# Kernel tuning notes

Measured on AMD Instinct MI355X. Metric: run time of the kernel, lower is better.

The kernel has to match this reference:

```python
import jax, jax.numpy as jnp
from jax import lax
import numpy as np

# Straight-through-estimator sign (standard BNN binarization):
# fwd: sign(x) with sign(0)=+1; bwd: pass gradient where |x|<=1 (hardtanh STE).
@jax.custom_vjp
def sign_ste(x):
    return jnp.where(x >= 0, 1.0, -1.0).astype(x.dtype)

def _sign_fwd(x):
    return sign_ste(x), x

def _sign_bwd(x, g):
    return (g * (jnp.abs(x) <= 1.0).astype(g.dtype),)

sign_ste.defvjp(_sign_fwd, _sign_bwd)

EPS = 1e-5  # BatchNorm eps (torch default)

def bn4(x, g, b):  # BatchNorm2d, training-mode batch stats, x: [N,C,H,W]
    m = x.mean((0, 2, 3), keepdims=True)
    v = x.var((0, 2, 3), keepdims=True)
    return g[None, :, None, None] * (x - m) * lax.rsqrt(v + EPS) + b[None, :, None, None]

def bn1(x, g, b):  # BatchNorm1d, x: [N,C]
    m = x.mean(0, keepdims=True)
    v = x.var(0, keepdims=True)
    return g * (x - m) * lax.rsqrt(v + EPS) + b

def bconv(x, W, b, first):
    # BinarizedConv2d: binarize weights always; binarize input except first layer.
    xb = x if first else sign_ste(x)
    y = lax.conv_general_dilated(xb, sign_ste(W), (1, 1), [(1, 1), (1, 1)],
                                 dimension_numbers=('NCHW', 'OIHW', 'NCHW'))
    return y + b[None, :, None, None]

def maxpool2(x):
    return lax.reduce_window(x, -jnp.inf, lax.max, (1, 1, 2, 2), (1, 1, 2, 2), 'VALID')

def ht(x):  # Hardtanh
    return jnp.clip(x, -1.0, 1.0)

CONV_CH = [(3, 64), (64, 128), (128, 256), (256, 256), (256, 512), (512, 512), (512, 512), (512, 512)]
LIN_CH = [(512, 512), (512, 512), (512, 10)]
POOL_AFTER = (0, 1, 3, 5, 7)  # conv indices followed by MaxPool2d

def setup_inputs():
    key = jax.random.key(0)
    ks = iter(jax.random.split(key, 64))
    d = {"x": jax.random.normal(next(ks), (256, 3, 32, 32), jnp.float32)}
    for i, (ci, co) in enumerate(CONV_CH):
        d[f"cw{i}"] = jax.random.normal(next(ks), (co, ci, 3, 3), jnp.float32) * 0.1
        d[f"cb{i}"] = jnp.zeros((co,), jnp.float32)
        d[f"cg{i}"] = jnp.ones((co,), jnp.float32)
        d[f"ct{i}"] = jnp.zeros((co,), jnp.float32)
    for i, (ci, co) in enumerate(LIN_CH):
        d[f"lw{i}"] = jax.random.normal(next(ks), (co, ci), jnp.float32) * 0.1
        d[f"lb{i}"] = jnp.zeros((co,), jnp.float32)
        d[f"lg{i}"] = jnp.ones((co,), jnp.float32)
        d[f"lt{i}"] = jnp.zeros((co,), jnp.float32)
    return d

def _forward(x, cw, cb, cg, ct, lw, lb, lg, lt):
    h = x
    for i in range(8):
        h = bconv(h, cw[i], cb[i], i == 0)
        if i in POOL_AFTER:
            h = maxpool2(h)
        h = ht(bn4(h, cg[i], ct[i]))
    h = h.reshape(h.shape[0], -1)  # [N, 512] after 5 pools on 32x32
    for i in range(3):
        h = sign_ste(h) @ sign_ste(lw[i]).T + lb[i]  # BinarizedLinear
        h = bn1(h, lg[i], lt[i])
        if i < 2:
            h = ht(h)  # Dropout is identity in eval mode
    return jax.nn.log_softmax(h, axis=-1)

def reference(x,
              cw0, cb0, cg0, ct0, cw1, cb1, cg1, ct1, cw2, cb2, cg2, ct2,
              cw3, cb3, cg3, ct3, cw4, cb4, cg4, ct4, cw5, cb5, cg5, ct5,
              cw6, cb6, cg6, ct6, cw7, cb7, cg7, ct7,
              lw0, lb0, lg0, lt0, lw1, lb1, lg1, lt1, lw2, lb2, lg2, lt2):
    cw = [cw0, cw1, cw2, cw3, cw4, cw5, cw6, cw7]
    cb = [cb0, cb1, cb2, cb3, cb4, cb5, cb6, cb7]
    cg = [cg0, cg1, cg2, cg3, cg4, cg5, cg6, cg7]
    ct = [ct0, ct1, ct2, ct3, ct4, ct5, ct6, ct7]
    lw = [lw0, lw1, lw2]
    lb = [lb0, lb1, lb2]
    lg = [lg0, lg1, lg2]
    lt = [lt0, lt1, lt2]
    return _forward(x, cw, cb, cg, ct, lw, lb, lg, lt)
```

## Files before the change

### kernel.cpp

```cpp
#include <hip/hip_runtime.h>
#include <hip/hip_bf16.h>

typedef unsigned long long u64;

#define EPSV 1e-5

__device__ __forceinline__ int imax(int a, int b) { return a > b ? a : b; }
__device__ __forceinline__ int iclamp(int v, int lo, int hi) { return v < lo ? lo : (v > hi ? hi : v); }

struct PrepArgs {
    const float* src[10];
    u64* dst[10];
    int CW[10];
    int Co[10];
    int taps[10];
    int rowbase[11];
    u64* accs;
    int naccs;
};

__global__ __launch_bounds__(256) void prep_kernel(PrepArgs a) {
    __shared__ float buf[4608];
    const int blk = blockIdx.x;
    int z = blk * 19 + threadIdx.x;
    if (threadIdx.x < 19 && z < a.naccs) a.accs[z] = 0ULL;

    int l = 0;
    while (l < 9 && blk >= a.rowbase[l + 1]) ++l;
    const int row = blk - a.rowbase[l];
    const int CW = a.CW[l];
    const int taps = a.taps[l];
// ... 86 lines not shown
        double t1 = 0.0, t2 = 0.0;
#pragma unroll
        for (int r = 0; r < 4; ++r) { t1 += sh1[r][threadIdx.x]; t2 += sh2[r][threadIdx.x]; }
        double* sh = dacc + (size_t)(blockIdx.x & 7) * 1024;
        atomicAdd(&sh[2 * threadIdx.x], t1);
        atomicAdd(&sh[2 * threadIdx.x + 1], t2);
    }
}

__global__ __launch_bounds__(256) void bnpack_i(const short* __restrict__ in,
                                                const u64* __restrict__ iacc,
                                                const float* __restrict__ g,
                                                const float* __restrict__ b,
                                                u64* __restrict__ act, int Co, int wshift,
                                                int count) {
    __shared__ int2 sthr[520];
    for (int i = threadIdx.x; i < Co; i += 256) {
        long long S1 = 0, S2 = 0;
#pragma unroll
        for (int s = 0; s < 8; ++s) {
            S1 += (long long)iacc[s * 1024 + 2 * i];
            S2 += (long long)iacc[s * 1024 + 2 * i + 1];
        }
        double m = (double)S1 / count;
        double var = (double)S2 / count - m * m;
        double sc = (double)g[i] / sqrt(var + EPSV);
        int2 r;
        if (sc == 0.0) r = make_int2(b[i] >= 0.f ? (int)0x80000000 : 0x7fffffff, 0);
        else {
            double t = m - (double)b[i] / sc;
            if (t > 1.0e9) t = 1.0e9;
            if (t < -1.0e9) t = -1.0e9;
            r = (sc > 0.0) ? make_int2((int)ceil(t), 0) : make_int2((int)floor(t), 1);
        }
        sthr[(i >> 6) * 65 + (i & 63)] = r;
    }
    __syncthreads();
    int tid = blockIdx.x * 256 + threadIdx.x;
    int part = tid & 3;
    int word = tid >> 2;
    int w = word & ((1 << wshift) - 1);
    int pix = word >> wshift;
    const int4* r4 = (const int4*)(in + (size_t)pix * Co + (w << 6) + part * 16);
    u64 bits = 0;
#pragma unroll
    for (int q = 0; q < 2; ++q) {
        int4 v = r4[q];
        int words4[4] = {v.x, v.y, v.z, v.w};
#pragma unroll
        for (int u = 0; u < 4; ++u) {
#pragma unroll
            for (int h = 0; h < 2; ++h) {
                int c = part * 16 + q * 8 + u * 2 + h;
                int val = (int)(short)((h == 0) ? (words4[u] & 0xffff) : ((unsigned)words4[u] >> 16));
                int2 t = sthr[w * 65 + c];
                bool bit = t.y ? (val <= t.x) : (val >= t.x);
                bits |= (u64)bit << c;
            }
        }
    }
    bits |= __shfl_xor(bits, 1);
    bits |= __shfl_xor(bits, 2);
    if (part == 0) act[word] = bits;
}

template <int CW, int HIN, bool POOL, int WC, bool INTERIOR>
__device__ __forceinline__ void row_accum(const u64* __restrict__ inb,
                                          const u64* __restrict__ wpkT, int Co, int co,
                                          const int* yoff, const bool* ry, int* cnt) {
    constexpr int HP = POOL ? HIN / 2 : HIN;
    constexpr int WS = POOL ? 4 : 3;
    constexpr int NA = POOL ? 4 : 1;
#pragma unroll 1
    for (int w0 = 0; w0 < CW; w0 += WC) {
        u64 wg[9 * WC];
#pragma unroll
        for (int k = 0; k < 9; ++k)
#pragma unroll
            for (int w = 0; w < WC; ++w)
                wg[k * WC + w] = wpkT[(size_t)(k * CW + w0 + w) * Co + co];
        u64 cur[WS][WS][WC];
#pragma unroll
        for (int d = 0; d < WS; ++d) {
            int cc = d - 1;
            int ccc = cc < 0 ? 0 : cc;
#pragma unroll
            for (int r = 0; r < WS; ++r) {
                const u64* p = inb + yoff[r] + ccc * CW + w0;
                if (WC == 1) {
                    cur[r][d][0] = p[0];
                } else {
                    ulonglong2 v = *(const ulonglong2*)p;
                    cur[r][d][0] = v.x;
                    cur[r][d][1] = v.y;
                }
            }
        }
#pragma unroll
        for (int xp = 0; xp < HP; ++xp) {
            if constexpr (POOL) {
#pragma unroll
                for (int py = 0; py < 2; ++py)
#pragma unroll
                    for (int qx = 0; qx < 2; ++qx)
#pragma unroll
                        for (int ky = 0; ky < 3; ++ky)
#pragma unroll
                            for (int kx = 0; kx < 3; ++kx) {
                                int d = qx + kx;
                                int cc = 2 * xp + d - 1;
                                if (cc >= 0 && cc < HIN) {
#pragma unroll
                                    for (int w = 0; w < WC; ++w) {
                                        int pc = (int)__popcll(cur[py + ky][d][w] ^
                                                               wg[(ky * 3 + kx) * WC + w]);
                                        if constexpr (INTERIOR)
                                            cnt[xp * NA + py * 2 + qx] += pc;
                                        else
                                            cnt[xp * NA + py * 2 + qx] += ry[py + ky] ? pc : 0;
                                    }
                                }
                            }
            } else {
#pragma unroll
                for (int ky = 0; ky < 3; ++ky)
#pragma unroll
                    for (int kx = 0; kx < 3; ++kx) {
                        int cc = xp + kx - 1;
                        if (cc >= 0 && cc < HIN) {
#pragma unroll
                            for (int w = 0; w < WC; ++w) {
                                int pc = (int)__popcll(cur[ky][kx][w] ^
                                                       wg[(ky * 3 + kx) * WC + w]);
                                if constexpr (INTERIOR)
                                    cnt[xp] += pc;
                                else
                                    cnt[xp] += ry[ky] ? pc : 0;
                            }
                        }
                    }
            }
            if (xp < HP - 1) {
                if constexpr (POOL) {
#pragma unroll
                    for (int r = 0; r < WS; ++r)
#pragma unroll
                        for (int w = 0; w < WC; ++w) {
                            cur[r][0][w] = cur[r][2][w];
                            cur[r][1][w] = cur[r][3][w];
                        }
#pragma unroll
                    for (int dd = 2; dd < 4; ++dd) {
                        int cc = 2 * (xp + 1) + dd - 1;
                        int ccc = cc >= HIN ? HIN - 1 : cc;
#pragma unroll
                        for (int r = 0; r < WS; ++r) {
                            const u64* p = inb + yoff[r] + ccc * CW + w0;
                            if (WC == 1) {
                                cur[r][dd][0] = p[0];
                            } else {
                                ulonglong2 v = *(const ulonglong2*)p;
                                cur[r][dd][0] = v.x;
                                cur[r][dd][1] = v.y;
                            }
                        }
                    }
                } else {
#pragma unroll
                    for (int r = 0; r < WS; ++r)
#pragma unroll
                        for (int w = 0; w < WC; ++w) {
                            cur[r][0][w] = cur[r][1][w];
                            cur[r][1][w] = cur[r][2][w];
                        }
                    int cc = xp + 2;
                    int ccc = cc >= HIN ? HIN - 1 : cc;
#pragma unroll
                    for (int r = 0; r < WS; ++r) {
                        const u64* p = inb + yoff[r] + ccc * CW + w0;
                        if (WC == 1) {
                            cur[r][2][0] = p[0];
                        } else {
                            ulonglong2 v = *(const ulonglong2*)p;
                            cur[r][2][0] = v.x;
                            cur[r][2][1] = v.y;
                        }
                    }
                }
            }
        }
    }
}

template <int CW, int HIN, bool POOL, int WC, bool FIRST>
__global__ __launch_bounds__(256) void bconv_row_f(const void* __restrict__ inprev,
                                                   const void* __restrict__ pstats,
                                                   const float* __restrict__ pg,
                                                   const float* __restrict__ pb, int pcount,
                                                   const u64* __restrict__ wpkT,
                                                   short* __restrict__ out,
                                                   u64* __restrict__ iacc, int Co) {
    constexpr int HP = POOL ? HIN / 2 : HIN;
    constexpr int WS = POOL ? 4 : 3;
    constexpr int NA = POOL ? 4 : 1;
    constexpr int ROWS = POOL ? 10 : 6;
    constexpr int Ci = CW * 64;
    __shared__ __align__(16) u64 sU[ROWS * HIN * CW];
    __shared__ int2 sthr[CW * 65];
    __shared__ float2 sthf[64];

    if constexpr (FIRST) {
        if (threadIdx.x < 64) {
            const double* dacc = (const double*)pstats;
            int i = threadIdx.x;
// ... 3 lines not shown
                S1 += dacc[s * 1024 + 2 * i];
                S2 += dacc[s * 1024 + 2 * i + 1];
            }
            double m = S1 / pcount;
            double var = S2 / pcount - m * m;
            double sc = (double)pg[i] / sqrt(var + EPSV);
            float2 r;
            if (sc == 0.0) r = make_float2(pb[i] >= 0.f ? -3.0e38f : 3.0e38f, 1.f);
            else {
                double t = m - (double)pb[i] / sc;
                r = make_float2((float)t, sc > 0.0 ? 1.f : -1.f);
            }
            sthf[i] = r;
        }
    } else {
        const u64* pacc = (const u64*)pstats;
        for (int i = threadIdx.x; i < Ci; i += 256) {
            long long S1 = 0, S2 = 0;
#pragma unroll
            for (int s = 0; s < 8; ++s) {
                S1 += (long long)pacc[s * 1024 + 2 * i];
                S2 += (long long)pacc[s * 1024 + 2 * i + 1];
            }
            double m = (double)S1 / pcount;
            double var = (double)S2 / pcount - m * m;
            double sc = (double)pg[i] / sqrt(var + EPSV);
            int2 r;
            if (sc == 0.0) r = make_int2(pb[i] >= 0.f ? (int)0x80000000 : 0x7fffffff, 0);
            else {
                double t = m - (double)pb[i] / sc;
                if (t > 1.0e9) t = 1.0e9;
                if (t < -1.0e9) t = -1.0e9;
                r = (sc > 0.0) ? make_int2((int)ceil(t), 0) : make_int2((int)floor(t), 1);
            }
            sthr[(i >> 6) * 65 + (i & 63)] = r;
        }
    }
    __syncthreads();

    const int bi = blockIdx.x;
    constexpr int BPN = HP / 4;
    const int n = bi / BPN;
    const int yp0 = (bi % BPN) * 4;
    const int ylo = imax(0, (POOL ? 2 * yp0 : yp0) - 1);
    const int yhiU = POOL ? (2 * yp0 + 8) : (yp0 + 4);
    const int yhi = yhiU > HIN - 1 ? HIN - 1 : yhiU;
    const int nrows = yhi - ylo + 1;
    const int nw = nrows * HIN * CW;

    if constexpr (FIRST) {
        const float* src = (const float*)inprev;
        for (int t = threadIdx.x; t < nw; t += 256) {
            int x = t % HIN;
            int yr = t / HIN;
            int y = ylo + yr;
            const float4* p = (const float4*)(src + (size_t)((n * 16 + y) * 16 + x) * 64);
            u64 bits = 0;
#pragma unroll
// ... 111 lines not shown
}

template <int CW, int HIN, bool POOL>
__global__ __launch_bounds__(256) void bconv_tiny_f(const short* __restrict__ inprev,
                                                    const u64* __restrict__ pacc,
                                                    const float* __restrict__ pg,
                                                    const float* __restrict__ pb, int pcount,
                                                    const u64* __restrict__ wpkT,
                                                    short* __restrict__ out,
                                                    u64* __restrict__ iacc, int Co) {
    constexpr int NPX = HIN * HIN;
    constexpr int HP = POOL ? HIN / 2 : HIN;
    constexpr int Ci = CW * 64;
    __shared__ int2 sthr[CW * 65];
    __shared__ u64 sU[4][NPX * CW];

    for (int i = threadIdx.x; i < Ci; i += 256) {
        long long S1 = 0, S2 = 0;
#pragma unroll
        for (int s = 0; s < 8; ++s) {
            S1 += (long long)pacc[s * 1024 + 2 * i];
            S2 += (long long)pacc[s * 1024 + 2 * i + 1];
        }
        double m = (double)S1 / pcount;
        double var = (double)S2 / pcount - m * m;
        double sc = (double)pg[i] / sqrt(var + EPSV);
        int2 r;
        if (sc == 0.0) r = make_int2(pb[i] >= 0.f ? (int)0x80000000 : 0x7fffffff, 0);
        else {
            double t = m - (double)pb[i] / sc;
            if (t > 1.0e9) t = 1.0e9;
            if (t < -1.0e9) t = -1.0e9;
            r = (sc > 0.0) ? make_int2((int)ceil(t), 0) : make_int2((int)floor(t), 1);
        }
        sthr[(i >> 6) * 65 + (i & 63)] = r;
    }
    __syncthreads();

    const int nbase = blockIdx.x * 4;
    for (int t = threadIdx.x; t < 4 * NPX * CW; t += 256) {
        int img = t / (NPX * CW);
        int rem = t % (NPX * CW);
        int w = rem % CW;
        int i = rem / CW;
        const int4* p = (const int4*)(inprev + (size_t)((nbase + img) * NPX + i) * Ci + w * 64);
        u64 bits = 0;
#pragma unroll
        for (int q = 0; q < 8; ++q) {
            int4 v = p[q];
            int wd[4] = {v.x, v.y, v.z, v.w};
#pragma unroll
            for (int u = 0; u < 4; ++u) {
#pragma unroll
                for (int h = 0; h < 2; ++h) {
                    int j = q * 8 + u * 2 + h;
                    int val = (int)(short)((h == 0) ? (wd[u] & 0xffff) : ((unsigned)wd[u] >> 16));
                    int2 th = sthr[w * 65 + j];
                    bool bit = th.y ? (val <= th.x) : (val >= th.x);
// ... 153 lines not shown
    __syncthreads();
    float z[10];
#pragma unroll
    for (int o = 0; o < 10; ++o) {
        double S1 = w1[0][o] + w1[1][o] + w1[2][o] + w1[3][o];
        double S2 = w2[0][o] + w2[1][o] + w2[2][o] + w2[3][o];
        double m = S1 / 256.0;
        double var = S2 / 256.0 - m * m;
        float sm = (float)m;
        float siv = (float)(1.0 / sqrt(var + EPSV));
        z[o] = g[o] * (v[o] - sm) * siv + bta[o];
    }
    float mx = z[0];
#pragma unroll
    for (int o = 1; o < 10; ++o) mx = fmaxf(mx, z[o]);
    float se = 0.f;
#pragma unroll
    for (int o = 0; o < 10; ++o) se += expf(z[o] - mx);
    float ls = logf(se);
#pragma unroll
    for (int o = 0; o < 10; ++o) out[n * 10 + o] = z[o] - mx - ls;
}

extern "C" void kernel_launch(void* const* d_in, const int* in_sizes, int n_in, void* d_out,
                              int out_size, void* d_ws, size_t ws_size, hipStream_t stream) {
    (void)in_sizes; (void)n_in; (void)out_size; (void)ws_size;
    const float* x = (const float*)d_in[0];
    const float *cw[8], *cb[8], *cg[8], *ct[8];
    for (int i = 0; i < 8; ++i) {
        cw[i] = (const float*)d_in[1 + 4 * i];
        cb[i] = (const float*)d_in[2 + 4 * i];
        cg[i] = (const float*)d_in[3 + 4 * i];
        ct[i] = (const float*)d_in[4 + 4 * i];
    }
    const float *lw[3], *lb[3], *lg[3], *lt[3];
    for (int i = 0; i < 3; ++i) {
        lw[i] = (const float*)d_in[33 + 4 * i];
        lb[i] = (const float*)d_in[34 + 4 * i];
        lg[i] = (const float*)d_in[35 + 4 * i];
        lt[i] = (const float*)d_in[36 + 4 * i];
    }

    static const int CIs[8] = {3, 64, 128, 256, 256, 512, 512, 512};
    static const int COs[8] = {64, 128, 256, 256, 512, 512, 512, 512};

    char* ws = (char*)d_ws;
    size_t off = 0;
    auto alloc = [&](size_t bytes) -> void* {
        void* p = ws + off;
        off += (bytes + 255) & ~(size_t)255;
        return p;
    };

    u64* accs = (u64*)alloc((size_t)8 * 8 * 1024 * 8);
    u64* fcs0 = (u64*)alloc(2048 * 8);
    u64* fcs1 = (u64*)alloc(2048 * 8);
    double* dacc0 = (double*)accs;
    auto iacc = [&](int layer) { return accs + (size_t)layer * 8192; };

    u64* wpkT[8] = {};
    for (int i = 1; i < 8; ++i) wpkT[i] = (u64*)alloc((size_t)COs[i] * 9 * (CIs[i] / 64) * 8);
    u64* wpl[3];
    int LO[3] = {512, 512, 10};
    for (int i = 0; i < 3; ++i) wpl[i] = (u64*)alloc((size_t)LO[i] * 8 * 8);
    u64* act7 = (u64*)alloc((size_t)256 * 8 * 8);
    float* out0 = (float*)alloc((size_t)65536 * 64 * 4);
    short* i16A = (short*)alloc((size_t)16384 * 256 * 2);
    short* i16B = (short*)alloc((size_t)16384 * 256 * 2);

    PrepArgs pa;
    int rb = 0;
    for (int i = 1; i < 8; ++i) {
        int e = i - 1;
        pa.src[e] = cw[i];
        pa.dst[e] = wpkT[i];
        pa.CW[e] = CIs[i] / 64;
        pa.Co[e] = COs[i];
        pa.taps[e] = 9;
        pa.rowbase[e] = rb;
        rb += COs[i];
    }
    for (int i = 0; i < 3; ++i) {
        int e = 7 + i;
        pa.src[e] = lw[i];
        pa.dst[e] = wpl[i];
        pa.CW[e] = 8;
        pa.Co[e] = LO[i];
        pa.taps[e] = 1;
        pa.rowbase[e] = rb;
        rb += LO[i];
    }
    pa.rowbase[10] = rb;
    pa.accs = accs;
    pa.naccs = 8 * 8 * 1024 + 2048 + 2048;
    prep_kernel<<<rb, 256, 0, stream>>>(pa);

    conv0_lane<<<2048, 256, 0, stream>>>(x, cw[0], out0, dacc0);

    bconv_row_f<1, 16, true, 1, true><<<dim3(512, 2), 256, 0, stream>>>(
        out0, dacc0, cg[0], ct[0], 65536, wpkT[1], i16A, iacc(1), 128);

    bconv_row_f<2, 8, false, 2, false><<<dim3(512, 4), 256, 0, stream>>>(
        i16A, iacc(1), cg[1], ct[1], 16384, wpkT[2], i16B, iacc(2), 256);

    bconv_row_f<4, 8, true, 2, false><<<dim3(256, 4), 256, 0, stream>>>(
        i16B, iacc(2), cg[2], ct[2], 16384, wpkT[3], i16A, iacc(3), 256);

    bconv_row_f<4, 4, false, 2, false><<<dim3(256, 8), 256, 0, stream>>>(
        i16A, iacc(3), cg[3], ct[3], 4096, wpkT[4], i16B, iacc(4), 512);

    bconv_tiny_f<8, 4, true><<<dim3(64, 8), 256, 0, stream>>>(
        i16B, iacc(4), cg[4], ct[4], 4096, wpkT[5], i16A, iacc(5), 512);

    bconv_tiny_f<8, 2, false><<<dim3(64, 8), 256, 0, stream>>>(
        i16A, iacc(5), cg[5], ct[5], 1024, wpkT[6], i16B, iacc(6), 512);

    bconv_tiny_f<8, 2, true><<<dim3(64, 8), 256, 0, stream>>>(
        i16B, iacc(6), cg[6], ct[6], 1024, wpkT[7], i16A, iacc(7), 512);

    bnpack_i<<<32, 256, 0, stream>>>(i16A, iacc(7), cg[7], ct[7], act7, 512, 3, 256);

    lin_kernel<<<512, 256, 0, stream>>>(act7, wpl[0], lb[0], lg[0], lt[0], fcs0);
    lin_kernel<<<512, 256, 0, stream>>>(fcs0, wpl[1], lb[1], lg[1], lt[1], fcs1);
    lin2_lsm<<<1, 256, 0, stream>>>(fcs1, wpl[2], lb[2], lg[2], lt[2], (float*)d_out);
}
```

Measured before the change: 405.9 us.

## Fuse all layer kernels into one cooperative persistent mega-kernel with grid syncs

Replaces the chain of about a dozen kernel launches (weight prep, conv layers, bn-pack, linear layers, log-softmax) with a single cooperative kernel. It loops persistent blocks over virtual tiles and uses grid-wide syncs between stages, keeping the old launch sequence as a fallback. The goal is to remove per-launch overhead and the idle tails between stages. In exchange, the grid is capped at 512 blocks sized by occupancy, which can leave big layers under-parallelized, and grid sync has its own cost. The 128-bit vector loads in row_accum are also replaced with two scalar loads.

```diff
diff --git a/kernel.cpp b/kernel.cpp
--- a/kernel.cpp
+++ b/kernel.cpp
@@ -1,5 +1,7 @@
 #include <hip/hip_runtime.h>
-#include <hip/hip_bf16.h>
+#include <hip/hip_cooperative_groups.h>
+
+namespace cg = cooperative_groups;
 
 typedef unsigned long long u64;
 
@@ -7,6 +9,147 @@
 
 __device__ __forceinline__ int imax(int a, int b) { return a > b ? a : b; }
 __device__ __forceinline__ int iclamp(int v, int lo, int hi) { return v < lo ? lo : (v > hi ? hi : v); }
+
+__device__ __forceinline__ int2 thr_int(long long S1, long long S2, float gv, float bv, int count) {
+    double m = (double)S1 / count;
+    double var = (double)S2 / count - m * m;
+    double sc = (double)gv / sqrt(var + EPSV);
+    int2 r;
+    if (sc == 0.0) r = make_int2(bv >= 0.f ? (int)0x80000000 : 0x7fffffff, 0);
+    else {
+        double t = m - (double)bv / sc;
+        if (t > 1.0e9) t = 1.0e9;
+        if (t < -1.0e9) t = -1.0e9;
+        r = (sc > 0.0) ? make_int2((int)ceil(t), 0) : make_int2((int)floor(t), 1);
+    }
+    return r;
+}
+
+template <int CW, int HIN, bool POOL, int WC, bool INTERIOR>
+__device__ __forceinline__ void row_accum(const u64* __restrict__ inb,
+                                          const u64* __restrict__ wpkT, int Co, int co,
+                                          const int* yoff, const bool* ry, int* cnt) {
+    constexpr int HP = POOL ? HIN / 2 : HIN;
+    constexpr int WS = POOL ? 4 : 3;
+    constexpr int NA = POOL ? 4 : 1;
+#pragma unroll 1
+    for (int w0 = 0; w0 < CW; w0 += WC) {
+        u64 wg[9 * WC];
+#pragma unroll
+        for (int k = 0; k < 9; ++k)
+#pragma unroll
+            for (int w = 0; w < WC; ++w)
+                wg[k * WC + w] = wpkT[(size_t)(k * CW + w0 + w) * Co + co];
+        u64 cur[WS][WS][WC];
+#pragma unroll
+        for (int d = 0; d < WS; ++d) {
+            int cc = d - 1;
+            int ccc = cc < 0 ? 0 : cc;
+#pragma unroll
+            for (int r = 0; r < WS; ++r) {
+                const u64* p = inb + yoff[r] + ccc * CW + w0;
+                if (WC == 1) {
+                    cur[r][d][0] = p[0];
+                } else {
+                    cur[r][d][0] = p[0];
+                    cur[r][d][1] = p[1];
+                }
+            }
+        }
+#pragma unroll
+        for (int xp = 0; xp < HP; ++xp) {
+            if constexpr (POOL) {
+#pragma unroll
+                for (int py = 0; py < 2; ++py)
+#pragma unroll
+                    for (int qx = 0; qx < 2; ++qx)
+#pragma unroll
+                        for (int ky = 0; ky < 3; ++ky)
+#pragma unroll
+                            for (int kx = 0; kx < 3; ++kx) {
+                                int d = qx + kx;
+                                int cc = 2 * xp + d - 1;
+                                if (cc >= 0 && cc < HIN) {
+#pragma unroll
+                                    for (int w = 0; w < WC; ++w) {
+                                        int pc = (int)__popcll(cur[py + ky][d][w] ^
+                                                               wg[(ky * 3 + kx) * WC + w]);
+                                        if constexpr (INTERIOR)
+                                            cnt[xp * NA + py * 2 + qx] += pc;
+                                        else
+                                            cnt[xp * NA + py * 2 + qx] += ry[py + ky] ? pc : 0;
+                                    }
+                                }
+                            }
+            } else {
+#pragma unroll
+                for (int ky = 0; ky < 3; ++ky)
+#pragma unroll
+                    for (int kx = 0; kx < 3; ++kx) {
+                        int cc = xp + kx - 1;
+                        if (cc >= 0 && cc < HIN) {
+#pragma unroll
+                            for (int w = 0; w < WC; ++w) {
+                                int pc = (int)__popcll(cur[ky][kx][w] ^
+                                                       wg[(ky * 3 + kx) * WC + w]);
+                                if constexpr (INTERIOR)
+                                    cnt[xp] += pc;
+                                else
+                                    cnt[xp] += ry[ky] ? pc : 0;
+                            }
+                        }
+                    }
+            }
+            if (xp < HP - 1) {
+                if constexpr (POOL) {
+#pragma unroll
+                    for (int r = 0; r < WS; ++r)
+#pragma unroll
+                        for (int w = 0; w < WC; ++w) {
+                            cur[r][0][w] = cur[r][2][w];
+                            cur[r][1][w] = cur[r][3][w];
+                        }
+#pragma unroll
+                    for (int dd = 2; dd < 4; ++dd) {
+                        int cc = 2 * (xp + 1) + dd - 1;
+                        int ccc = cc >= HIN ? HIN - 1 : cc;
+#pragma unroll
+                        for (int r = 0; r < WS; ++r) {
+                            const u64* p = inb + yoff[r] + ccc * CW + w0;
+                            if (WC == 1) {
+                                cur[r][dd][0] = p[0];
+                            } else {
+                                cur[r][dd][0] = p[0];
+                                cur[r][dd][1] = p[1];
+                            }
+                        }
+                    }
+                } else {
+#pragma unroll
+                    for (int r = 0; r < WS; ++r)
+#pragma unroll
+                        for (int w = 0; w < WC; ++w) {
+                            cur[r][0][w] = cur[r][1][w];
+                            cur[r][1][w] = cur[r][2][w];
+                        }
+                    int cc = xp + 2;
+                    int ccc = cc >= HIN ? HIN - 1 : cc;
+#pragma unroll
+                    for (int r = 0; r < WS; ++r) {
+                        const u64* p = inb + yoff[r] + ccc * CW + w0;
+                        if (WC == 1) {
+                            cur[r][2][0] = p[0];
+                        } else {
+                            cur[r][2][0] = p[0];
+                            cur[r][2][1] = p[1];
+                        }
+                    }
+                }
+            }
+        }
+    }
+}
+
 
 struct PrepArgs {
     const float* src[10];
@@ -139,18 +282,7 @@
             S1 += (long long)iacc[s * 1024 + 2 * i];
             S2 += (long long)iacc[s * 1024 + 2 * i + 1];
         }
-        double m = (double)S1 / count;
-        double var = (double)S2 / count - m * m;
-        double sc = (double)g[i] / sqrt(var + EPSV);
-        int2 r;
-        if (sc == 0.0) r = make_int2(b[i] >= 0.f ? (int)0x80000000 : 0x7fffffff, 0);
-        else {
-            double t = m - (double)b[i] / sc;
-            if (t > 1.0e9) t = 1.0e9;
-            if (t < -1.0e9) t = -1.0e9;
-            r = (sc > 0.0) ? make_int2((int)ceil(t), 0) : make_int2((int)floor(t), 1);
-        }
-        sthr[(i >> 6) * 65 + (i & 63)] = r;
+        sthr[(i >> 6) * 65 + (i & 63)] = thr_int(S1, S2, g[i], b[i], count);
     }
     __syncthreads();
     int tid = blockIdx.x * 256 + threadIdx.x;
@@ -179,134 +311,6 @@
     bits |= __shfl_xor(bits, 1);
     bits |= __shfl_xor(bits, 2);
     if (part == 0) act[word] = bits;
-}
-
-template <int CW, int HIN, bool POOL, int WC, bool INTERIOR>
-__device__ __forceinline__ void row_accum(const u64* __restrict__ inb,
-                                          const u64* __restrict__ wpkT, int Co, int co,
-                                          const int* yoff, const bool* ry, int* cnt) {
-    constexpr int HP = POOL ? HIN / 2 : HIN;
-    constexpr int WS = POOL ? 4 : 3;
-    constexpr int NA = POOL ? 4 : 1;
-#pragma unroll 1
-    for (int w0 = 0; w0 < CW; w0 += WC) {
-        u64 wg[9 * WC];
-#pragma unroll
-        for (int k = 0; k < 9; ++k)
-#pragma unroll
-            for (int w = 0; w < WC; ++w)
-                wg[k * WC + w] = wpkT[(size_t)(k * CW + w0 + w) * Co + co];
-        u64 cur[WS][WS][WC];
-#pragma unroll
-        for (int d = 0; d < WS; ++d) {
-            int cc = d - 1;
-            int ccc = cc < 0 ? 0 : cc;
-#pragma unroll
-            for (int r = 0; r < WS; ++r) {
-                const u64* p = inb + yoff[r] + ccc * CW + w0;
-                if (WC == 1) {
-                    cur[r][d][0] = p[0];
-                } else {
-                    ulonglong2 v = *(const ulonglong2*)p;
-                    cur[r][d][0] = v.x;
-                    cur[r][d][1] = v.y;
-                }
-            }
-        }
-#pragma unroll
-        for (int xp = 0; xp < HP; ++xp) {
-            if constexpr (POOL) {
-#pragma unroll
-                for (int py = 0; py < 2; ++py)
-#pragma unroll
-                    for (int qx = 0; qx < 2; ++qx)
-#pragma unroll
-                        for (int ky = 0; ky < 3; ++ky)
-#pragma unroll
-                            for (int kx = 0; kx < 3; ++kx) {
-                                int d = qx + kx;
-                                int cc = 2 * xp + d - 1;
-                                if (cc >= 0 && cc < HIN) {
-#pragma unroll
-                                    for (int w = 0; w < WC; ++w) {
-                                        int pc = (int)__popcll(cur[py + ky][d][w] ^
-                                                               wg[(ky * 3 + kx) * WC + w]);
-                                        if constexpr (INTERIOR)
-                                            cnt[xp * NA + py * 2 + qx] += pc;
-                                        else
-                                            cnt[xp * NA + py * 2 + qx] += ry[py + ky] ? pc : 0;
-                                    }
-                                }
-                            }
-            } else {
-#pragma unroll
-                for (int ky = 0; ky < 3; ++ky)
-#pragma unroll
-                    for (int kx = 0; kx < 3; ++kx) {
-                        int cc = xp + kx - 1;
-                        if (cc >= 0 && cc < HIN) {
-#pragma unroll
-                            for (int w = 0; w < WC; ++w) {
-                                int pc = (int)__popcll(cur[ky][kx][w] ^
-                                                       wg[(ky * 3 + kx) * WC + w]);
-                                if constexpr (INTERIOR)
-                                    cnt[xp] += pc;
-                                else
-                                    cnt[xp] += ry[ky] ? pc : 0;
-                            }
-                        }
-                    }
-            }
-            if (xp < HP - 1) {
-                if constexpr (POOL) {
-#pragma unroll
-                    for (int r = 0; r < WS; ++r)
-#pragma unroll
-                        for (int w = 0; w < WC; ++w) {
-                            cur[r][0][w] = cur[r][2][w];
-                            cur[r][1][w] = cur[r][3][w];
-                        }
-#pragma unroll
-                    for (int dd = 2; dd < 4; ++dd) {
-                        int cc = 2 * (xp + 1) + dd - 1;
-                        int ccc = cc >= HIN ? HIN - 1 : cc;
-#pragma unroll
-                        for (int r = 0; r < WS; ++r) {
-                            const u64* p = inb + yoff[r] + ccc * CW + w0;
-                            if (WC == 1) {
-                                cur[r][dd][0] = p[0];
-                            } else {
-                                ulonglong2 v = *(const ulonglong2*)p;
-                                cur[r][dd][0] = v.x;
-                                cur[r][dd][1] = v.y;
-                            }
-                        }
-                    }
-                } else {
-#pragma unroll
-                    for (int r = 0; r < WS; ++r)
-#pragma unroll
-                        for (int w = 0; w < WC; ++w) {
-                            cur[r][0][w] = cur[r][1][w];
-                            cur[r][1][w] = cur[r][2][w];
-                        }
-                    int cc = xp + 2;
-                    int ccc = cc >= HIN ? HIN - 1 : cc;
-#pragma unroll
-                    for (int r = 0; r < WS; ++r) {
-                        const u64* p = inb + yoff[r] + ccc * CW + w0;
-                        if (WC == 1) {
-                            cur[r][2][0] = p[0];
-                        } else {
-                            ulonglong2 v = *(const ulonglong2*)p;
-                            cur[r][2][0] = v.x;
-                            cur[r][2][1] = v.y;
-                        }
-                    }
-                }
-            }
-        }
-    }
 }
 
 template <int CW, int HIN, bool POOL, int WC, bool FIRST>
@@ -356,18 +360,7 @@
                 S1 += (long long)pacc[s * 1024 + 2 * i];
                 S2 += (long long)pacc[s * 1024 + 2 * i + 1];
             }
-            double m = (double)S1 / pcount;
-            double var = (double)S2 / pcount - m * m;
-            double sc = (double)pg[i] / sqrt(var + EPSV);
-            int2 r;
-            if (sc == 0.0) r = make_int2(pb[i] >= 0.f ? (int)0x80000000 : 0x7fffffff, 0);
-            else {
-                double t = m - (double)pb[i] / sc;
-                if (t > 1.0e9) t = 1.0e9;
-                if (t < -1.0e9) t = -1.0e9;
-                r = (sc > 0.0) ? make_int2((int)ceil(t), 0) : make_int2((int)floor(t), 1);
-            }
-            sthr[(i >> 6) * 65 + (i & 63)] = r;
+            sthr[(i >> 6) * 65 + (i & 63)] = thr_int(S1, S2, pg[i], pb[i], pcount);
         }
     }
     __syncthreads();
@@ -525,18 +518,7 @@
             S1 += (long long)pacc[s * 1024 + 2 * i];
             S2 += (long long)pacc[s * 1024 + 2 * i + 1];
         }
-        double m = (double)S1 / pcount;
-        double var = (double)S2 / pcount - m * m;
-        double sc = (double)pg[i] / sqrt(var + EPSV);
-        int2 r;
-        if (sc == 0.0) r = make_int2(pb[i] >= 0.f ? (int)0x80000000 : 0x7fffffff, 0);
-        else {
-            double t = m - (double)pb[i] / sc;
-            if (t > 1.0e9) t = 1.0e9;
-            if (t < -1.0e9) t = -1.0e9;
-            r = (sc > 0.0) ? make_int2((int)ceil(t), 0) : make_int2((int)floor(t), 1);
-        }
-        sthr[(i >> 6) * 65 + (i & 63)] = r;
+        sthr[(i >> 6) * 65 + (i & 63)] = thr_int(S1, S2, pg[i], pb[i], pcount);
     }
     __syncthreads();
 
@@ -736,14 +718,636 @@
     for (int o = 0; o < 10; ++o) out[n * 10 + o] = z[o] - mx - ls;
 }
 
+
+struct MegaArgs {
+    const float* psrc[10];
+    u64* pdst[10];
+    int pCW[10];
+    int pCo[10];
+    int ptaps[10];
+    int prow[11];
+    u64* accs;
+    int naccs;
+    const float* x;
+    const float* cw0;
+    float* out0;
+    const float* cg[8];
+    const float* ct[8];
+    u64* wpkT[8];
+    short* i16A;
+    short* i16B;
+    u64* act7;
+    u64* wpl[3];
+    const float* lb[3];
+    const float* lg[3];
+    const float* lt[3];
+    u64* fcs0;
+    u64* fcs1;
+    float* out;
+};
+
+template <int CW, int HIN, bool POOL, int WC, bool FIRST, int NBX, int NBY>
+__device__ void bconv_row_stage(const void* inprev, const void* pstats,
+                                const float* pg, const float* pb, int pcount,
+                                const u64* __restrict__ wpkT, short* __restrict__ out,
+                                u64* __restrict__ iacc, int Co, char* smem) {
+    constexpr int HP = POOL ? HIN / 2 : HIN;
+    constexpr int WS = POOL ? 4 : 3;
+    constexpr int NA = POOL ? 4 : 1;
+    constexpr int Ci = CW * 64;
+    int2* sthr = (int2*)smem;
+    float2* sthf = (float2*)smem;
+    u64* sU = (u64*)(smem + 4608);
+    u64* sacc = (u64*)(smem + 7680);
+
+    if constexpr (FIRST) {
+        if (threadIdx.x < 64) {
+            const double* dacc = (const double*)pstats;
+            int i = threadIdx.x;
+            double S1 = 0.0, S2 = 0.0;
+#pragma unroll
+            for (int s = 0; s < 8; ++s) {
+                S1 += dacc[s * 1024 + 2 * i];
+                S2 += dacc[s * 1024 + 2 * i + 1];
+            }
+            double m = S1 / pcount;
+            double var = S2 / pcount - m * m;
+            double sc = (double)pg[i] / sqrt(var + EPSV);
+            float2 r;
+            if (sc == 0.0) r = make_float2(pb[i] >= 0.f ? -3.0e38f : 3.0e38f, 1.f);
+            else {
+                double t = m - (double)pb[i] / sc;
+                r = make_float2((float)t, sc > 0.0 ? 1.f : -1.f);
+            }
+            sthf[i] = r;
+        }
+    } else {
+        const u64* pacc = (const u64*)pstats;
+        for (int i = threadIdx.x; i < Ci; i += 256) {
+            long long S1 = 0, S2 = 0;
+#pragma unroll
+            for (int s = 0; s < 8; ++s) {
+                S1 += (long long)pacc[s * 1024 + 2 * i];
+                S2 += (long long)pacc[s * 1024 + 2 * i + 1];
+            }
+            sthr[(i >> 6) * 65 + (i & 63)] = thr_int(S1, S2, pg[i], pb[i], pcount);
+        }
+    }
+
+    for (int vb = blockIdx.x; vb < NBX * NBY; vb += gridDim.x) {
+        __syncthreads();
+        const int bx = vb % NBX;
+        const int by = vb / NBX;
+        constexpr int BPN = HP / 4;
+        const int n = bx / BPN;
+        const int yp0 = (bx % BPN) * 4;
+        const int ylo = imax(0, (POOL ? 2 * yp0 : yp0) - 1);
+        const int yhiU = POOL ? (2 * yp0 + 8) : (yp0 + 4);
+        const int yhi = yhiU > HIN - 1 ? HIN - 1 : yhiU;
+        const int nrows = yhi - ylo + 1;
+        const int nw = nrows * HIN * CW;
+
+        if constexpr (FIRST) {
+            const float* src = (const float*)inprev;
+            for (int t = threadIdx.x; t < nw; t += 256) {
+                int x = t % HIN;
+                int yr = t / HIN;
+                int y = ylo + yr;
+                const float4* p = (const float4*)(src + (size_t)((n * 16 + y) * 16 + x) * 64);
+                u64 bits = 0;
+#pragma unroll
+                for (int q = 0; q < 16; ++q) {
+                    float4 v = p[q];
+                    float vv[4] = {v.x, v.y, v.z, v.w};
+#pragma unroll
+                    for (int u = 0; u < 4; ++u) {
+                        int c = q * 4 + u;
+                        float2 th = sthf[c];
+                        bool bit = (th.y > 0.f) ? (vv[u] >= th.x) : (vv[u] <= th.x);
+                        bits |= (u64)bit << c;
+                    }
+                }
+                sU[t] = bits;
+            }
+        } else {
+            const short* src = (const short*)inprev;
+            for (int t = threadIdx.x; t < nw; t += 256) {
+                int w = t % CW;
+                int x = (t / CW) % HIN;
+                int yr = t / (HIN * CW);
+                int y = ylo + yr;
+                const int4* p = (const int4*)(src + (size_t)((n * HIN + y) * HIN + x) * Ci + w * 64);
+                u64 bits = 0;
+#pragma unroll
+                for (int q = 0; q < 8; ++q) {
+                    int4 v = p[q];
+                    int wd[4] = {v.x, v.y, v.z, v.w};
+#pragma unroll
+                    for (int u = 0; u < 4; ++u) {
+#pragma unroll
+                        for (int h = 0; h < 2; ++h) {
+                            int j = q * 8 + u * 2 + h;
+                            int val = (int)(short)((h == 0) ? (wd[u] & 0xffff)
+                                                            : ((unsigned)wd[u] >> 16));
+                            int2 th = sthr[w * 65 + j];
+                            bool bit = th.y ? (val <= th.x) : (val >= th.x);
+                            bits |= (u64)bit << j;
+                        }
+                    }
+                }
+                sU[t] = bits;
+            }
+        }
+        __syncthreads();
+
+        const int lane = threadIdx.x & 63;
+        const int wave = threadIdx.x >> 6;
+        const int co = by * 64 + lane;
+        const int yp = yp0 + wave;
+        const int grow = n * HP + yp;
+        const int y0 = (POOL ? 2 * yp : yp) - 1;
+        int yoff[WS];
+        bool ry[WS];
+#pragma unroll
+        for (int r = 0; r < WS; ++r) {
+            int y = y0 + r;
+            ry[r] = (unsigned)y < (unsigned)HIN;
+            int yc = iclamp(y, 0, HIN - 1);
+            yoff[r] = (yc - ylo) * (HIN * CW);
+        }
+        int cnt[HP * NA];
+#pragma unroll
+        for (int i = 0; i < HP * NA; ++i) cnt[i] = 0;
+
+        if (yp > 0 && yp < HP - 1)
+            row_accum<CW, HIN, POOL, WC, true>(sU, wpkT, Co, co, yoff, ry, cnt);
+        else
+            row_accum<CW, HIN, POOL, WC, false>(sU, wpkT, Co, co, yoff, ry, cnt);
+
+        const int nr0 = (int)ry[0] + (int)ry[1] + (int)ry[2];
+        const int nr1 = POOL ? ((int)ry[1] + (int)ry[2] + (int)ry[WS - 1]) : 0;
+
+        int s1 = 0;
+        long long s2 = 0;
+        short* orow = out + (size_t)grow * HP * Co + co;
+#pragma unroll
+        for (int xp = 0; xp < HP; ++xp) {
+            int ival;
+            if constexpr (POOL) {
+                int best = -2147483647;
+#pragma unroll
+                for (int py = 0; py < 2; ++py) {
+                    const int nrv = py ? nr1 : nr0;
+#pragma unroll
+                    for (int qx = 0; qx < 2; ++qx) {
+                        int ncols = 3;
+                        if (xp == 0 && qx == 0) ncols = 2;
+                        if (xp == HP - 1 && qx == 1) ncols = 2;
+                        int v = 64 * CW * nrv * ncols - 2 * cnt[xp * NA + py * 2 + qx];
+                        best = imax(best, v);
+                    }
+                }
+                ival = best;
+            } else {
+                const int ncols = (xp == 0 || xp == HIN - 1) ? 2 : 3;
+                ival = 64 * CW * nr0 * ncols - 2 * cnt[xp];
+            }
+            orow[(size_t)xp * Co] = (short)ival;
+            s1 += ival;
+            s2 += (long long)ival * ival;
+        }
+
+        if (threadIdx.x < 128) sacc[threadIdx.x] = 0ULL;
+        __syncthreads();
+        atomicAdd(&sacc[lane], (u64)(long long)s1);
+        atomicAdd(&sacc[64 + lane], (u64)s2);
+        __syncthreads();
+        u64* sh = iacc + (size_t)(bx & 7) * 1024;
+        if (threadIdx.x < 64)
+            atomicAdd(&sh[2 * (by * 64 + threadIdx.x)], sacc[threadIdx.x]);
+        else if (threadIdx.x < 128)
+            atomicAdd(&sh[2 * (by * 64 + threadIdx.x - 64) + 1], sacc[threadIdx.x]);
+    }
+}
+
+template <int CW, int HIN, bool POOL>
+__device__ void bconv_tiny_stage(const short* __restrict__ inprev, const u64* __restrict__ pacc,
+                                 const float* pg, const float* pb, int pcount,
+                                 const u64* __restrict__ wpkT, short* __restrict__ out,
+                                 u64* __restrict__ iacc, int Co, char* smem) {
+    constexpr int NPX = HIN * HIN;
+    constexpr int HP = POOL ? HIN / 2 : HIN;
+    constexpr int Ci = CW * 64;
+    int2* sthr = (int2*)smem;
+    u64* sU = (u64*)(smem + 4608);
+    u64* sacc = (u64*)(smem + 8704);
+
+    for (int i = threadIdx.x; i < Ci; i += 256) {
+        long long S1 = 0, S2 = 0;
+#pragma unroll
+        for (int s = 0; s < 8; ++s) {
+            S1 += (long long)pacc[s * 1024 + 2 * i];
+            S2 += (long long)pacc[s * 1024 + 2 * i + 1];
+        }
+        sthr[(i >> 6) * 65 + (i & 63)] = thr_int(S1, S2, pg[i], pb[i], pcount);
+    }
+
+    for (int vb = blockIdx.x; vb < 512; vb += gridDim.x) {
+        __syncthreads();
+        const int bx = vb & 63;
+        const int by = vb >> 6;
+        const int nbase = bx * 4;
+        for (int t = threadIdx.x; t < 4 * NPX * CW; t += 256) {
+            int img = t / (NPX * CW);
+            int rem = t % (NPX * CW);
+            int w = rem % CW;
+            int i = rem / CW;
+            const int4* p = (const int4*)(inprev + (size_t)((nbase + img) * NPX + i) * Ci + w * 64);
+            u64 bits = 0;
+#pragma unroll
+            for (int q = 0; q < 8; ++q) {
+                int4 v = p[q];
+                int wd[4] = {v.x, v.y, v.z, v.w};
+#pragma unroll
+                for (int u = 0; u < 4; ++u) {
+#pragma unroll
+                    for (int h = 0; h < 2; ++h) {
+                        int j = q * 8 + u * 2 + h;
+                        int val = (int)(short)((h == 0) ? (wd[u] & 0xffff) : ((unsigned)wd[u] >> 16));
+                        int2 th = sthr[w * 65 + j];
+                        bool bit = th.y ? (val <= th.x) : (val >= th.x);
+                        bits |= (u64)bit << j;
+                    }
+                }
+            }
+            sU[(size_t)img * (NPX * CW) + i * CW + w] = bits;
+        }
+        __syncthreads();
+
+        const int lane = threadIdx.x & 63;
+        const int co = by * 64 + lane;
+        const int n = nbase + (threadIdx.x >> 6);
+        const u64* inb = sU + (size_t)(threadIdx.x >> 6) * (NPX * CW);
+        int cnt[NPX];
+#pragma unroll
+        for (int i = 0; i < NPX; ++i) cnt[i] = 0;
+
+#pragma unroll 2
+        for (int w = 0; w < CW; ++w) {
+            u64 win[NPX];
+#pragma unroll
+            for (int i = 0; i < NPX; ++i) win[i] = inb[i * CW + w];
+#pragma unroll
+            for (int k = 0; k < 9; ++k) {
+                u64 wb = wpkT[(size_t)(k * CW + w) * Co + co];
+                const int ky = k / 3, kx = k % 3;
+#pragma unroll
+                for (int py = 0; py < HIN; ++py)
+#pragma unroll
+                    for (int px = 0; px < HIN; ++px) {
+                        const int yy = py + ky - 1, xx = px + kx - 1;
+                        if (yy >= 0 && yy < HIN && xx >= 0 && xx < HIN)
+                            cnt[py * HIN + px] += (int)__popcll(win[yy * HIN + xx] ^ wb);
+                    }
+            }
+        }
+
+        int fin[NPX];
+#pragma unroll
+        for (int py = 0; py < HIN; ++py)
+#pragma unroll
+            for (int px = 0; px < HIN; ++px) {
+                const int nk = ((py == 0 || py == HIN - 1) ? 2 : 3) *
+                               ((px == 0 || px == HIN - 1) ? 2 : 3);
+                fin[py * HIN + px] = 64 * CW * nk - 2 * cnt[py * HIN + px];
+            }
+
+        short vals[HP * HP];
+        if constexpr (POOL) {
+#pragma unroll
+            for (int py = 0; py < HP; ++py)
+#pragma unroll
+                for (int px = 0; px < HP; ++px)
+                    vals[py * HP + px] = (short)imax(
+                        imax(fin[(2 * py) * HIN + 2 * px], fin[(2 * py) * HIN + 2 * px + 1]),
+                        imax(fin[(2 * py + 1) * HIN + 2 * px],
+                             fin[(2 * py + 1) * HIN + 2 * px + 1]));
+        } else {
+#pragma unroll
+            for (int i = 0; i < NPX; ++i) vals[i] = (short)fin[i];
+        }
+#pragma unroll
+        for (int p = 0; p < HP * HP; ++p) out[(size_t)(n * HP * HP + p) * Co + co] = vals[p];
+
+        long long s1 = 0, s2 = 0;
+#pragma unroll
+        for (int p = 0; p < HP * HP; ++p) {
+            s1 += vals[p];
+            s2 += (long long)vals[p] * vals[p];
+        }
+        if (threadIdx.x < 128) sacc[threadIdx.x] = 0ULL;
+        __syncthreads();
+        atomicAdd(&sacc[lane], (u64)s1);
+        atomicAdd(&sacc[64 + lane], (u64)s2);
+        __syncthreads();
+        u64* sh = iacc + (size_t)(bx & 7) * 1024;
+        if (threadIdx.x < 64)
+            atomicAdd(&sh[2 * (by * 64 + threadIdx.x)], sacc[threadIdx.x]);
+        else if (threadIdx.x < 128)
+            atomicAdd(&sh[2 * (by * 64 + threadIdx.x - 64) + 1], sacc[threadIdx.x]);
+    }
+}
+
+__device__ void lin_stage(const u64* __restrict__ hp, const u64* __restrict__ wp,
+                          const float* lb, const float* g, const float* bta,
+                          u64* __restrict__ op, char* smem) {
+    double* sh1 = (double*)smem;
+    double* sh2 = (double*)(smem + 2048);
+    float* smf = (float*)(smem + 4096);
+    const int n = threadIdx.x;
+    for (int o = blockIdx.x; o < 512; o += gridDim.x) {
+        __syncthreads();
+        const u64* hr = hp + n * 8;
+        const u64* wr = wp + o * 8;
+        int s = 0;
+#pragma unroll
+        for (int w = 0; w < 8; ++w) s += (int)__popcll(hr[w] ^ wr[w]);
+        float val = (float)(512 - 2 * s) + lb[o];
+        sh1[n] = (double)val;
+        sh2[n] = (double)val * (double)val;
+        __syncthreads();
+        for (int st = 128; st > 0; st >>= 1) {
+            if (n < st) {
+                sh1[n] += sh1[n + st];
+                sh2[n] += sh2[n + st];
+            }
+            __syncthreads();
+        }
+        if (n == 0) {
+            double m = sh1[0] / 256.0;
+            double var = sh2[0] / 256.0 - m * m;
+            smf[0] = (float)m;
+            smf[1] = (float)(1.0 / sqrt(var + EPSV));
+        }
+        __syncthreads();
+        float zz = g[o] * (val - smf[0]) * smf[1] + bta[o];
+        if (zz >= 0.f) atomicOr(&op[(size_t)n * 8 + (o >> 6)], 1ULL << (o & 63));
+    }
+}
+
+__global__ __launch_bounds__(256, 2) void mega_kernel(MegaArgs A) {
+    cg::grid_group gg = cg::this_grid();
+    __shared__ __align__(16) char smem[18432];
+    const int lane = threadIdx.x & 63;
+    const int wave = threadIdx.x >> 6;
+
+    for (int vb = blockIdx.x; vb < A.prow[10]; vb += gridDim.x) {
+        __syncthreads();
+        int z = vb * 19 + threadIdx.x;
+        if (threadIdx.x < 19 && z < A.naccs) A.accs[z] = 0ULL;
+        int l = 0;
+        while (l < 9 && vb >= A.prow[l + 1]) ++l;
+        const int row = vb - A.prow[l];
+        const int CW = A.pCW[l];
+        const int taps = A.ptaps[l];
+        const int nf = CW * 64 * taps;
+        float* buf = (float*)smem;
+        const float* srow = A.psrc[l] + (size_t)row * nf;
+        for (int i = threadIdx.x; i < nf; i += 256) buf[i] = srow[i];
+        __syncthreads();
+        const int t = threadIdx.x;
+        if (t < taps * CW) {
+            u64 bits = 0;
+            if (taps == 9) {
+                int k = t % 9, w = t / 9;
+                for (int j = 0; j < 64; ++j) bits |= (u64)(buf[(w * 64 + j) * 9 + k] >= 0.f) << j;
+                A.pdst[l][(size_t)(k * CW + w) * A.pCo[l] + row] = bits;
+            } else {
+                for (int j = 0; j < 64; ++j) bits |= (u64)(buf[t * 64 + j] >= 0.f) << j;
+                A.pdst[l][(size_t)row * CW + t] = bits;
+            }
+        }
+    }
+    gg.sync();
+
+    {
+        float ws[27];
+#pragma unroll
+        for (int j = 0; j < 27; ++j) ws[j] = (A.cw0[lane * 27 + j] >= 0.f) ? 1.f : -1.f;
+        float* simg = (float*)smem;
+        double* sh1 = (double*)(smem + 4096);
+        double* sh2 = (double*)(smem + 6144);
+        double* dacc0 = (double*)A.accs;
+        for (int vb = blockIdx.x; vb < 2048; vb += gridDim.x) {
+            __syncthreads();
+            const int gp0 = vb * 32;
+            const int n = gp0 >> 8;
+            const int ypA = (gp0 >> 4) & 15;
+            const int yb = 2 * ypA - 1;
+            const float* xb = A.x + (size_t)n * 3072;
+            for (int t = threadIdx.x; t < 612; t += 256) {
+                int ci = t / 204;
+                int rem = t % 204;
+                int r = rem / 34;
+                int ccv = rem % 34;
+                int yy = yb + r;
+                int xx = ccv - 1;
+                float v = 0.f;
+                if ((unsigned)yy < 32u && (unsigned)xx < 32u) v = xb[(ci * 32 + yy) * 32 + xx];
+                simg[(ci * 6 + r) * 34 + ccv] = v;
+            }
+            __syncthreads();
+            double s1 = 0.0, s2 = 0.0;
+#pragma unroll 2
+            for (int pi = 0; pi < 8; ++pi) {
+                const int lp = wave * 8 + pi;
+                const int gp = gp0 + lp;
+                const int xp = lp & 15;
+                const int rbase = 2 * (lp >> 4);
+                const int cbase = 2 * xp;
+                float win[3][4][4];
+#pragma unroll
+                for (int ci = 0; ci < 3; ++ci)
+#pragma unroll
+                    for (int r = 0; r < 4; ++r)
+#pragma unroll
+                        for (int c = 0; c < 4; ++c)
+                            win[ci][r][c] = simg[(ci * 6 + rbase + r) * 34 + cbase + c];
+                float a00 = 0.f, a01 = 0.f, a10 = 0.f, a11 = 0.f;
+#pragma unroll
+                for (int ci = 0; ci < 3; ++ci)
+#pragma unroll
+                    for (int ky = 0; ky < 3; ++ky)
+#pragma unroll
+                        for (int kx = 0; kx < 3; ++kx) {
+                            float wv = ws[ci * 9 + ky * 3 + kx];
+                            a00 += win[ci][ky][kx] * wv;
+                            a01 += win[ci][ky][kx + 1] * wv;
+                            a10 += win[ci][ky + 1][kx] * wv;
+                            a11 += win[ci][ky + 1][kx + 1] * wv;
+                        }
+                float val = fmaxf(fmaxf(a00, a01), fmaxf(a10, a11));
+                A.out0[(size_t)gp * 64 + lane] = val;
+                s1 += (double)val;
+                s2 += (double)val * (double)val;
+            }
+            sh1[wave * 64 + lane] = s1;
+            sh2[wave * 64 + lane] = s2;
+            __syncthreads();
+            if (threadIdx.x < 64) {
+                double t1 = 0.0, t2 = 0.0;
+#pragma unroll
+                for (int r = 0; r < 4; ++r) {
+                    t1 += sh1[r * 64 + threadIdx.x];
+                    t2 += sh2[r * 64 + threadIdx.x];
+                }
+                double* sh = dacc0 + (size_t)(vb & 7) * 1024;
+                atomicAdd(&sh[2 * threadIdx.x], t1);
+                atomicAdd(&sh[2 * threadIdx.x + 1], t2);
+            }
+        }
+    }
+    gg.sync();
+
+    u64* iacc1 = A.accs + 1 * 8192;
+    u64* iacc2 = A.accs + 2 * 8192;
+    u64* iacc3 = A.accs + 3 * 8192;
+    u64* iacc4 = A.accs + 4 * 8192;
+    u64* iacc5 = A.accs + 5 * 8192;
+    u64* iacc6 = A.accs + 6 * 8192;
+    u64* iacc7 = A.accs + 7 * 8192;
+
+    bconv_row_stage<1, 16, true, 1, true, 512, 2>(A.out0, A.accs, A.cg[0], A.ct[0], 65536,
+                                                  A.wpkT[1], A.i16A, iacc1, 128, smem);
+    gg.sync();
+    bconv_row_stage<2, 8, false, 2, false, 512, 4>(A.i16A, iacc1, A.cg[1], A.ct[1], 16384,
+                                                   A.wpkT[2], A.i16B, iacc2, 256, smem);
+    gg.sync();
+    bconv_row_stage<4, 8, true, 2, false, 256, 4>(A.i16B, iacc2, A.cg[2], A.ct[2], 16384,
+                                                  A.wpkT[3], A.i16A, iacc3, 256, smem);
+    gg.sync();
+    bconv_row_stage<4, 4, false, 2, false, 256, 8>(A.i16A, iacc3, A.cg[3], A.ct[3], 4096,
+                                                   A.wpkT[4], A.i16B, iacc4, 512, smem);
+    gg.sync();
+    bconv_tiny_stage<8, 4, true>(A.i16B, iacc4, A.cg[4], A.ct[4], 4096, A.wpkT[5], A.i16A,
+                                 iacc5, 512, smem);
+    gg.sync();
+    bconv_tiny_stage<8, 2, false>(A.i16A, iacc5, A.cg[5], A.ct[5], 1024, A.wpkT[6], A.i16B,
+                                  iacc6, 512, smem);
+    gg.sync();
+    bconv_tiny_stage<8, 2, true>(A.i16B, iacc6, A.cg[6], A.ct[6], 1024, A.wpkT[7], A.i16A,
+                                 iacc7, 512, smem);
+    gg.sync();
+
+    {
+        int2* sthr = (int2*)smem;
+        for (int i = threadIdx.x; i < 512; i += 256) {
+            long long S1 = 0, S2 = 0;
+#pragma unroll
+            for (int s = 0; s < 8; ++s) {
+                S1 += (long long)iacc7[s * 1024 + 2 * i];
+                S2 += (long long)iacc7[s * 1024 + 2 * i + 1];
+            }
+            sthr[(i >> 6) * 65 + (i & 63)] = thr_int(S1, S2, A.cg[7][i], A.ct[7][i], 256);
+        }
+        __syncthreads();
+        for (int vb = blockIdx.x; vb < 32; vb += gridDim.x) {
+            int tid = vb * 256 + threadIdx.x;
+            int part = tid & 3;
+            int word = tid >> 2;
+            int w = word & 7;
+            int pix = word >> 3;
+            const int4* r4 = (const int4*)(A.i16A + (size_t)pix * 512 + (w << 6) + part * 16);
+            u64 bits = 0;
+#pragma unroll
+            for (int q = 0; q < 2; ++q) {
+                int4 v = r4[q];
+                int wd[4] = {v.x, v.y, v.z, v.w};
+#pragma unroll
+                for (int u = 0; u < 4; ++u) {
+#pragma unroll
+                    for (int h = 0; h < 2; ++h) {
+                        int c = part * 16 + q * 8 + u * 2 + h;
+                        int val = (int)(short)((h == 0) ? (wd[u] & 0xffff) : ((unsigned)wd[u] >> 16));
+                        int2 t = sthr[w * 65 + c];
+                        bool bit = t.y ? (val <= t.x) : (val >= t.x);
+                        bits |= (u64)bit << c;
+                    }
+                }
+            }
+            bits |= __shfl_xor(bits, 1);
+            bits |= __shfl_xor(bits, 2);
+            if (part == 0) A.act7[word] = bits;
+        }
+    }
+    gg.sync();
+
+    lin_stage(A.act7, A.wpl[0], A.lb[0], A.lg[0], A.lt[0], A.fcs0, smem);
+    gg.sync();
+    lin_stage(A.fcs0, A.wpl[1], A.lb[1], A.lg[1], A.lt[1], A.fcs1, smem);
+    gg.sync();
+
+    if (blockIdx.x == 0) {
+        double* w1 = (double*)smem;
+        double* w2 = (double*)(smem + 512);
+        const int n = threadIdx.x;
+        u64 h[8];
+#pragma unroll
+        for (int w = 0; w < 8; ++w) h[w] = A.fcs1[n * 8 + w];
+        float v[10];
+#pragma unroll
+        for (int o = 0; o < 10; ++o) {
+            int s = 0;
+#pragma unroll
+            for (int w = 0; w < 8; ++w) s += (int)__popcll(h[w] ^ A.wpl[2][o * 8 + w]);
+            v[o] = (float)(512 - 2 * s) + A.lb[2][o];
+        }
+#pragma unroll
+        for (int o = 0; o < 10; ++o) {
+            double a = (double)v[o];
+            double b = a * a;
+#pragma unroll
+            for (int off = 32; off > 0; off >>= 1) {
+                a += __shfl_xor(a, off);
+                b += __shfl_xor(b, off);
+            }
+            if (lane == 0) {
+                w1[wave * 10 + o] = a;
+                w2[wave * 10 + o] = b;
+            }
+        }
+        __syncthreads();
+        float z[10];
+#pragma unroll
+        for (int o = 0; o < 10; ++o) {
+            double S1 = w1[0 * 10 + o] + w1[1 * 10 + o] + w1[2 * 10 + o] + w1[3 * 10 + o];
+            double S2 = w2[0 * 10 + o] + w2[1 * 10 + o] + w2[2 * 10 + o] + w2[3 * 10 + o];
+            double m = S1 / 256.0;
+            double var = S2 / 256.0 - m * m;
+            float sm = (float)m;
+            float siv = (float)(1.0 / sqrt(var + EPSV));
+            z[o] = A.lg[2][o] * (v[o] - sm) * siv + A.lt[2][o];
+        }
+        float mx = z[0];
+#pragma unroll
+        for (int o = 1; o < 10; ++o) mx = fmaxf(mx, z[o]);
+        float se = 0.f;
+#pragma unroll
+        for (int o = 0; o < 10; ++o) se += expf(z[o] - mx);
+        float ls = logf(se);
+#pragma unroll
+        for (int o = 0; o < 10; ++o) A.out[n * 10 + o] = z[o] - mx - ls;
+    }
+}
+
+
 extern "C" void kernel_launch(void* const* d_in, const int* in_sizes, int n_in, void* d_out,
                               int out_size, void* d_ws, size_t ws_size, hipStream_t stream) {
     (void)in_sizes; (void)n_in; (void)out_size; (void)ws_size;
     const float* x = (const float*)d_in[0];
-    const float *cw[8], *cb[8], *cg[8], *ct[8];
+    const float *cw[8], *cg[8], *ct[8];
     for (int i = 0; i < 8; ++i) {
         cw[i] = (const float*)d_in[1 + 4 * i];
-        cb[i] = (const float*)d_in[2 + 4 * i];
         cg[i] = (const float*)d_in[3 + 4 * i];
         ct[i] = (const float*)d_in[4 + 4 * i];
     }
@@ -782,53 +1386,101 @@
     short* i16A = (short*)alloc((size_t)16384 * 256 * 2);
     short* i16B = (short*)alloc((size_t)16384 * 256 * 2);
 
-    PrepArgs pa;
+    MegaArgs A;
     int rb = 0;
     for (int i = 1; i < 8; ++i) {
         int e = i - 1;
-        pa.src[e] = cw[i];
-        pa.dst[e] = wpkT[i];
-        pa.CW[e] = CIs[i] / 64;
-        pa.Co[e] = COs[i];
-        pa.taps[e] = 9;
-        pa.rowbase[e] = rb;
+        A.psrc[e] = cw[i];
+        A.pdst[e] = wpkT[i];
+        A.pCW[e] = CIs[i] / 64;
+        A.pCo[e] = COs[i];
+        A.ptaps[e] = 9;
+        A.prow[e] = rb;
         rb += COs[i];
     }
     for (int i = 0; i < 3; ++i) {
         int e = 7 + i;
-        pa.src[e] = lw[i];
-        pa.dst[e] = wpl[i];
-        pa.CW[e] = 8;
-        pa.Co[e] = LO[i];
-        pa.taps[e] = 1;
-        pa.rowbase[e] = rb;
+        A.psrc[e] = lw[i];
+        A.pdst[e] = wpl[i];
+        A.pCW[e] = 8;
+        A.pCo[e] = LO[i];
+        A.ptaps[e] = 1;
+        A.prow[e] = rb;
         rb += LO[i];
     }
-    pa.rowbase[10] = rb;
+    A.prow[10] = rb;
+    A.accs = accs;
+    A.naccs = 8 * 8 * 1024 + 2048 + 2048;
+    A.x = x;
+    A.cw0 = cw[0];
+    for (int i = 0; i < 8; ++i) {
+        A.cg[i] = cg[i];
+        A.ct[i] = ct[i];
+    }
+    A.wpkT[0] = nullptr;
+    for (int i = 1; i < 8; ++i) A.wpkT[i] = wpkT[i];
+    A.i16A = i16A;
+    A.i16B = i16B;
+    A.act7 = act7;
+    for (int i = 0; i < 3; ++i) {
+        A.wpl[i] = wpl[i];
+        A.lb[i] = lb[i];
+        A.lg[i] = lg[i];
+        A.lt[i] = lt[i];
+    }
+    A.fcs0 = fcs0;
+    A.fcs1 = fcs1;
+    A.out = (float*)d_out;
+    A.out0 = out0;
+
+    static int coop_grid = -2;
+    if (coop_grid == -2) {
+        int occ = 0;
+        hipError_t qe = hipOccupancyMaxActiveBlocksPerMultiprocessor(
+            &occ, (const void*)mega_kernel, 256, 0);
+        if (qe == hipSuccess && occ >= 1) {
+            int g = occ * 256;
+            coop_grid = g > 512 ? 512 : g;
+        } else {
+            coop_grid = 0;
+        }
+    }
+    if (coop_grid >= 64) {
+        void* kargs[] = {(void*)&A};
+        hipError_t le = hipLaunchCooperativeKernel((void*)mega_kernel, dim3(coop_grid),
+                                                   dim3(256), kargs, 0, stream);
+        if (le == hipSuccess) return;
+        coop_grid = 0;
+    }
+
+    PrepArgs pa;
+    for (int e = 0; e < 10; ++e) {
+        pa.src[e] = A.psrc[e];
+        pa.dst[e] = A.pdst[e];
+        pa.CW[e] = A.pCW[e];
+        pa.Co[e] = A.pCo[e];
+        pa.taps[e] = A.ptaps[e];
+        pa.rowbase[e] = A.prow[e];
+    }
+    pa.rowbase[10] = A.prow[10];
     pa.accs = accs;
-    pa.naccs = 8 * 8 * 1024 + 2048 + 2048;
+    pa.naccs = A.naccs;
     prep_kernel<<<rb, 256, 0, stream>>>(pa);
 
     conv0_lane<<<2048, 256, 0, stream>>>(x, cw[0], out0, dacc0);
 
     bconv_row_f<1, 16, true, 1, true><<<dim3(512, 2), 256, 0, stream>>>(
         out0, dacc0, cg[0], ct[0], 65536, wpkT[1], i16A, iacc(1), 128);
-
     bconv_row_f<2, 8, false, 2, false><<<dim3(512, 4), 256, 0, stream>>>(
         i16A, iacc(1), cg[1], ct[1], 16384, wpkT[2], i16B, iacc(2), 256);
-
     bconv_row_f<4, 8, true, 2, false><<<dim3(256, 4), 256, 0, stream>>>(
         i16B, iacc(2), cg[2], ct[2], 16384, wpkT[3], i16A, iacc(3), 256);
-
     bconv_row_f<4, 4, false, 2, false><<<dim3(256, 8), 256, 0, stream>>>(
         i16A, iacc(3), cg[3], ct[3], 4096, wpkT[4], i16B, iacc(4), 512);
-
     bconv_tiny_f<8, 4, true><<<dim3(64, 8), 256, 0, stream>>>(
         i16B, iacc(4), cg[4], ct[4], 4096, wpkT[5], i16A, iacc(5), 512);
-
     bconv_tiny_f<8, 2, false><<<dim3(64, 8), 256, 0, stream>>>(
         i16A, iacc(5), cg[5], ct[5], 1024, wpkT[6], i16B, iacc(6), 512);
-
     bconv_tiny_f<8, 2, true><<<dim3(64, 8), 256, 0, stream>>>(
         i16B, iacc(6), cg[6], ct[6], 1024, wpkT[7], i16A, iacc(7), 512);
 
```

Result: slower. 893.3 us (+120.1%).
